# Performance work log

Hardware: AMD Instinct MI355X
Metric: run time of the kernel (lower is better)

The kernel has to match this reference:

```python
import jax, jax.numpy as jnp
import numpy as np

EPS = 1e-5
TAU = 0.1

def _bn(x, g, b):
    # BatchNorm1d in training mode: batch statistics (biased variance)
    mu = jnp.mean(x, axis=0, keepdims=True)
    var = jnp.var(x, axis=0, keepdims=True)
    return (x - mu) * jax.lax.rsqrt(var + EPS) * g + b

def setup_inputs():
    key = jax.random.key(0)
    ks = jax.random.split(key, 8)
    B, D, H, L, P, C, ND, NP = 32768, 2048, 1024, 384, 192, 10, 2, 2
    s = 0.02
    u = jax.random.uniform(ks[7], (B, NP), minval=1e-6, maxval=1.0 - 1e-6)
    return {
        'x': jax.random.normal(ks[0], (B, D), dtype=jnp.float32),
        'W_pre': jax.random.normal(ks[1], (H, D), dtype=jnp.float32) * s,
        'b_pre': jnp.zeros((H,), jnp.float32),
        'g_pre': jnp.ones((H,), jnp.float32),
        'be_pre': jnp.zeros((H,), jnp.float32),
        'W_disc': jax.random.normal(ks[2], (L, H), dtype=jnp.float32) * s,
        'b_disc': jnp.zeros((L,), jnp.float32),
        'g_disc': jnp.ones((L,), jnp.float32),
        'be_disc': jnp.zeros((L,), jnp.float32),
        'W_dfc': jax.random.normal(ks[3], (ND, L), dtype=jnp.float32) * s,
        'b_dfc': jnp.zeros((ND,), jnp.float32),
        'W_sw': jax.random.normal(ks[4], (NP, L), dtype=jnp.float32) * s,
        'b_sw': jnp.zeros((NP,), jnp.float32),
        'W1': jax.random.normal(ks[5], (NP, P, H), dtype=jnp.float32) * s,
        'b1': jnp.zeros((NP, P), jnp.float32),
        'W2': jax.random.normal(ks[6], (NP, C, P), dtype=jnp.float32) * s,
        'b2': jnp.zeros((NP, C), jnp.float32),
        'gumbel_noise': -jnp.log(-jnp.log(u)),
    }

def reference(x, W_pre, b_pre, g_pre, be_pre, W_disc, b_disc, g_disc, be_disc,
              W_dfc, b_dfc, W_sw, b_sw, W1, b1, W2, b2, gumbel_noise):
    # pre_classifier: Linear + BN + ReLU
    feature = jax.nn.relu(_bn(x @ W_pre.T + b_pre, g_pre, be_pre))
    # GRL is identity in forward
    dp = jax.nn.relu(_bn(feature @ W_disc.T + b_disc, g_disc, be_disc))
    dom = dp @ W_dfc.T + b_dfc                      # [B, num_domains]
    sw = jax.nn.relu(dp @ W_sw.T + b_sw)            # [B, n_partition]
    gum = jax.nn.softmax((sw + gumbel_noise) / TAU, axis=-1)  # soft gumbel-softmax
    idx = jnp.argmax(gum, axis=-1)                  # [B] routing decision
    # compute both (tiny) experts densely, then select per sample (faithful math,
    # avoids per-sample gather of full weight matrices)
    h_all = jax.nn.relu(jnp.einsum('bd,epd->bep', feature, W1) + b1)  # [B,E,P]
    o_all = jnp.einsum('bep,ecp->bec', h_all, W2) + b2                # [B,E,C]
    out = jnp.take_along_axis(o_all, idx[:, None, None], axis=1)[:, 0]  # [B,C]
    # original: sum_p gum[b,p] * stacked (stacked has one entry) == out * sum(gum)
    cop = out * jnp.sum(gum, axis=-1, keepdims=True)
    return cop, dom, idx
```

## Files before the change

### kernel.cpp

```cpp
#include <hip/hip_runtime.h>
#include <math.h>

#define kB 32768
#define kD 2048
#define kH 1024
#define kL 384
#define kP 192
#define kC 10
#define kNP 2
#define kND 2
#define kNCAT 768
#define kTAU 0.1f
#define kEPS 1e-5f
#define NPART 256
#define SCALE 64.0f
#define INV_SC2 (1.0f / 4096.0f)

typedef _Float16 f16x8 __attribute__((ext_vector_type(8)));
typedef _Float16 f16x4 __attribute__((ext_vector_type(4)));
typedef float f32x4 __attribute__((ext_vector_type(4)));

#define WAITVM4   asm volatile("s_waitcnt vmcnt(4)" ::: "memory")
#define WAITVM0   asm volatile("s_waitcnt vmcnt(0)" ::: "memory")
#define WAITLGKM0 asm volatile("s_waitcnt lgkmcnt(0)" ::: "memory")

__device__ __forceinline__ void gll16(const unsigned short* g, unsigned short* l)
{
    __builtin_amdgcn_global_load_lds(
        (const __attribute__((address_space(1))) unsigned int*)g,
        (__attribute__((address_space(3))) unsigned int*)l, 16, 0, 0);
}

__device__ __host__ __forceinline__ int wkey(int r)
{
    return (r & 1) | ((r & 2) << 1) | ((r & 4) >> 1);
}

__global__ __launch_bounds__(256)
void split_pack(const float* __restrict__ in, unsigned short* __restrict__ out, int K)
{
    const int row = blockIdx.x;
    const int t = threadIdx.x;
    const int s = wkey(row & 7);
    const float* ir = in + (size_t)row * K;
    unsigned short* orow = out + (size_t)row * (K * 2);
    for (int k0 = t * 4; k0 < K; k0 += 1024) {
        const float4 v = *(const float4*)&ir[k0];
        const float a0 = v.x * SCALE, a1 = v.y * SCALE, a2 = v.z * SCALE, a3 = v.w * SCALE;
        const _Float16 h0 = (_Float16)a0, h1 = (_Float16)a1, h2 = (_Float16)a2, h3 = (_Float16)a3;
        const _Float16 l0 = (_Float16)(a0 - (float)h0), l1 = (_Float16)(a1 - (float)h1);
        const _Float16 l2 = (_Float16)(a2 - (float)h2), l3 = (_Float16)(a3 - (float)h3);
        const f16x4 hi = {h0, h1, h2, h3};
        const f16x4 lo = {l0, l1, l2, l3};
        const int kb = k0 >> 5, kk = k0 & 31;
        const int c = kk >> 3, off = kk & 7;
        *(f16x4*)&orow[kb * 64 + ((c ^ s) << 3) + off]       = hi;
        *(f16x4*)&orow[kb * 64 + (((c ^ 4) ^ s) << 3) + off] = lo;
    }
}

template<int KDIM, int TILEN, bool BN>
__global__ __launch_bounds__(512, 1)
void gemm_fused(const float* __restrict__ Afp,
                const unsigned short* __restrict__ Bpk,
                const float* __restrict__ bnsc, const float* __restrict__ bnsh,
                float* __restrict__ C, const int N, const int gridX,
                float* __restrict__ psum, float* __restrict__ psumsq, const int statN)
{
    constexpr int NKB = KDIM / 32;
    constexpr int NI = TILEN / 64;
    constexpr int BG = TILEN / 64;
    __shared__ __align__(16) unsigned short As_[2][256 * 64];
    __shared__ __align__(16) unsigned short Bs_[2][TILEN * 64];
    __shared__ float sScL[BN ? KDIM : 1];
    __shared__ float sShL[BN ? KDIM : 1];

    const int t = threadIdx.x;
    const int lane = t & 63;
    const int w = t >> 6;
    const int wr = w >> 2, wc = w & 3;
    const int lr = lane & 15, lg = lane >> 4;
    const int ca = (lg ^ wkey(lane & 7)) * 8;

    const int nwg = gridDim.x;
    const int chunk = nwg >> 3;
    const int bid = blockIdx.x;
    const int logical = (bid & 7) * chunk + (bid >> 3);
    const int bx = logical % gridX, by = logical / gridX;
    const int m0 = by * 256, n0 = bx * TILEN;

    const int arow = t >> 1;
    const int akh = t & 1;
    const int skey = wkey(arow & 7);
    const int c0 = akh * 2, c1 = akh * 2 + 1;
    const float* aSrc = Afp + (size_t)(m0 + arow) * KDIM + akh * 16;

    const size_t bstride = (size_t)NKB * 64;
    const unsigned short* bG[BG];
    int bLoff[BG];
#pragma unroll
    for (int it = 0; it < BG; ++it) {
        const int Q = (w * BG + it) * 64 + lane;
        bG[it] = Bpk + (size_t)(n0 + (Q >> 3)) * bstride + (Q & 7) * 8;
        bLoff[it] = (w * BG + it) * 512;
    }

    f32x4 acc[8][NI];
#pragma unroll
    for (int mi = 0; mi < 8; ++mi)
#pragma unroll
        for (int ni = 0; ni < NI; ++ni) acc[mi][ni] = (f32x4){0.f, 0.f, 0.f, 0.f};

    float4 av0[4], av1[4];

    auto issueA = [&](float4 (&av)[4], int kb) {
        const int kt = kb * 32;
#pragma unroll
        for (int j = 0; j < 4; ++j)
            av[j] = *(const float4*)&aSrc[kt + j * 4];
    };

    auto gllB = [&](int kb, int buf) {
#pragma unroll
        for (int it = 0; it < BG; ++it)
            gll16(bG[it] + (size_t)kb * 64, &Bs_[buf][bLoff[it]]);
    };

    auto writeA = [&](const float4 (&av)[4], int buf, int tile) {
        const int kt = tile * 32 + akh * 16;
        float v[16];
#pragma unroll
        for (int j = 0; j < 4; ++j) {
            float4 a = av[j];
            if constexpr (BN) {
                const float4 sc = *(const float4*)&sScL[kt + j * 4];
                const float4 sh = *(const float4*)&sShL[kt + j * 4];
                a.x = fmaxf(fmaf(a.x, sc.x, sh.x), 0.f);
                a.y = fmaxf(fmaf(a.y, sc.y, sh.y), 0.f);
                a.z = fmaxf(fmaf(a.z, sc.z, sh.z), 0.f);
                a.w = fmaxf(fmaf(a.w, sc.w, sh.w), 0.f);
            } else {
                a.x *= SCALE; a.y *= SCALE; a.z *= SCALE; a.w *= SCALE;
            }
            v[j * 4 + 0] = a.x; v[j * 4 + 1] = a.y;
            v[j * 4 + 2] = a.z; v[j * 4 + 3] = a.w;
        }
        f16x8 hi[2], lo[2];
#pragma unroll
        for (int h = 0; h < 2; ++h)
#pragma unroll
            for (int i = 0; i < 8; ++i) {
                const float x = v[h * 8 + i];
                const _Float16 hh = (_Float16)x;
                hi[h][i] = hh;
                lo[h][i] = (_Float16)(x - (float)hh);
            }
        unsigned short* dst = &As_[buf][arow * 64];
        *(f16x8*)&dst[(c0 ^ skey) * 8]       = hi[0];
        *(f16x8*)&dst[(c1 ^ skey) * 8]       = hi[1];
        *(f16x8*)&dst[((c0 ^ 4) ^ skey) * 8] = lo[0];
        *(f16x8*)&dst[((c1 ^ 4) ^ skey) * 8] = lo[1];
    };

    auto body = [&](int kb, const float4 (&avW)[4], float4 (&avI)[4]) {
        const int cur = kb & 1, nxt = cur ^ 1;
        if (kb + 1 < NKB) {
            writeA(avW, nxt, kb + 1);
            gllB(kb + 1, nxt);
        }
        __builtin_amdgcn_sched_barrier(0);
        if (kb + 2 < NKB) issueA(avI, kb + 2);

        f16x8 bh[NI], bl[NI];
#pragma unroll
        for (int ni = 0; ni < NI; ++ni) {
            const unsigned short* bb = &Bs_[cur][(wc * (16 * NI) + ni * 16 + lr) * 64];
            bh[ni] = *(const f16x8*)&bb[ca];
            bl[ni] = *(const f16x8*)&bb[ca ^ 32];
        }
#pragma unroll
        for (int mi = 0; mi < 8; ++mi) {
            const unsigned short* ab = &As_[cur][(wr * 128 + mi * 16 + lr) * 64];
            const f16x8 ah = *(const f16x8*)&ab[ca];
            const f16x8 al = *(const f16x8*)&ab[ca ^ 32];
#pragma unroll
            for (int ni = 0; ni < NI; ++ni)
                acc[mi][ni] = __builtin_amdgcn_mfma_f32_16x16x32_f16(ah, bh[ni], acc[mi][ni], 0, 0, 0);
#pragma unroll
            for (int ni = 0; ni < NI; ++ni)
                acc[mi][ni] = __builtin_amdgcn_mfma_f32_16x16x32_f16(ah, bl[ni], acc[mi][ni], 0, 0, 0);
#pragma unroll
            for (int ni = 0; ni < NI; ++ni)
                acc[mi][ni] = __builtin_amdgcn_mfma_f32_16x16x32_f16(al, bh[ni], acc[mi][ni], 0, 0, 0);
        }
        if (kb + 1 < NKB) {
            if (kb + 2 < NKB) { WAITVM4; } else { WAITVM0; }
            WAITLGKM0;
            __builtin_amdgcn_sched_barrier(0);
            __builtin_amdgcn_s_barrier();
            __builtin_amdgcn_sched_barrier(0);
        }
    };

    if constexpr (BN) {
        if (t < KDIM / 4) {
            ((float4*)sScL)[t] = ((const float4*)bnsc)[t];
            ((float4*)sShL)[t] = ((const float4*)bnsh)[t];
        }
        __syncthreads();
    }
    issueA(av0, 0);
    gllB(0, 0);
    __builtin_amdgcn_sched_barrier(0);
    issueA(av1, 1);
    writeA(av0, 0, 0);
    WAITVM4;
    WAITLGKM0;
    __builtin_amdgcn_sched_barrier(0);
    __builtin_amdgcn_s_barrier();
    __builtin_amdgcn_sched_barrier(0);

    for (int kb = 0; kb < NKB; kb += 2) {
        body(kb,     av1, av0);
        body(kb + 1, av0, av1);
    }

#pragma unroll
    for (int mi = 0; mi < 8; ++mi)
#pragma unroll
        for (int j = 0; j < 4; ++j) {
            const int row = m0 + wr * 128 + mi * 16 + lg * 4 + j;
            float* cr = C + (size_t)row * N + n0 + wc * (16 * NI) + lr;
#pragma unroll
            for (int ni = 0; ni < NI; ++ni) cr[ni * 16] = acc[mi][ni][j];
        }

#pragma unroll
    for (int ni = 0; ni < NI; ++ni) {
        float s = 0.f, sq = 0.f;
#pragma unroll
        for (int mi = 0; mi < 8; ++mi)
#pragma unroll
            for (int j = 0; j < 4; ++j) {
                const float v = acc[mi][ni][j];
                s += v;
                sq = fmaf(v, v, sq);
            }
        s  += __shfl_xor(s, 16);  s  += __shfl_xor(s, 32);
        sq += __shfl_xor(sq, 16); sq += __shfl_xor(sq, 32);
        const int col = n0 + wc * (16 * NI) + ni * 16 + lr;
        if (lane < 16 && col < statN) {
            psum[(size_t)(by * 2 + wr) * statN + col]   = s;
            psumsq[(size_t)(by * 2 + wr) * statN + col] = sq;
        }
    }
}

__global__ __launch_bounds__(256)
void colstat_finalize(const float* __restrict__ psum, const float* __restrict__ psumsq,
                      int ncols, const float* __restrict__ g, const float* __restrict__ be,
                      float* __restrict__ scale, float* __restrict__ shift,
                      float inv_sc, float outsc)
{
    const int c = blockIdx.x * 256 + threadIdx.x;
    if (c >= ncols) return;
    float s = 0.f, sq = 0.f;
    for (int i = 0; i < NPART; ++i) {
        s  += psum[(size_t)i * ncols + c];
        sq += psumsq[(size_t)i * ncols + c];
    }
    const float mup = s * (1.f / kB);
    const float var = (sq * (1.f / kB) - mup * mup) * inv_sc * inv_sc;
    const float scl = outsc * g[c] * rsqrtf(var + kEPS) * inv_sc;
    scale[c] = scl;
    shift[c] = fmaf(-mup, scl, outsc * be[c]);
}

__global__ __launch_bounds__(256)
void tail_kernel(const float* __restrict__ Z2,
                 const float* __restrict__ scale2, const float* __restrict__ shift2,
                 const float* __restrict__ W_dfc, const float* __restrict__ b_dfc,
                 const float* __restrict__ W_sw, const float* __restrict__ b_sw,
                 const float* __restrict__ b1, const float* __restrict__ W2,
                 const float* __restrict__ b2, const float* __restrict__ noise,
                 float* __restrict__ out)
{
    __shared__ float sWdfc[kND * kL];
    __shared__ float sWsw[kNP * kL];
    __shared__ float sW2[kNP * kC * kP];
    __shared__ float sb1[kNP * kP];
    __shared__ float sScale[kL];
    __shared__ float sShift[kL];
    const int t = threadIdx.x;
    for (int i = t; i < kND * kL; i += 256) sWdfc[i] = W_dfc[i];
    for (int i = t; i < kNP * kL; i += 256) sWsw[i] = W_sw[i];
    for (int i = t; i < kNP * kC * kP; i += 256) sW2[i] = W2[i];
    for (int i = t; i < kNP * kP; i += 256) sb1[i] = b1[i];
    for (int i = t; i < kL; i += 256) { sScale[i] = scale2[i]; sShift[i] = shift2[i]; }
    __syncthreads();

    const int lane = t & 63;
    const int b = blockIdx.x * 4 + (t >> 6);
    const float* z = Z2 + (size_t)b * kNCAT;

    float d0 = 0.f, d1 = 0.f, s0 = 0.f, s1 = 0.f;
#pragma unroll
    for (int j = 0; j < 6; ++j) {
        const int k = lane + j * 64;
        const float dp = fmaxf(fmaf(z[k], sScale[k], sShift[k]), 0.f);
        d0 = fmaf(dp, sWdfc[k],      d0);
        d1 = fmaf(dp, sWdfc[kL + k], d1);
        s0 = fmaf(dp, sWsw[k],       s0);
        s1 = fmaf(dp, sWsw[kL + k],  s1);
    }
#pragma unroll
    for (int off = 32; off; off >>= 1) {
        d0 += __shfl_xor(d0, off);
        d1 += __shfl_xor(d1, off);
        s0 += __shfl_xor(s0, off);
        s1 += __shfl_xor(s1, off);
    }
    d0 += b_dfc[0];
    d1 += b_dfc[1];

    const float sw0 = fmaxf(s0 + b_sw[0], 0.f);
    const float sw1 = fmaxf(s1 + b_sw[1], 0.f);
    const float l0 = (sw0 + noise[(size_t)b * 2 + 0]) * (1.f / kTAU);
    const float l1 = (sw1 + noise[(size_t)b * 2 + 1]) * (1.f / kTAU);
    const float mx = fmaxf(l0, l1);
    const float e0 = expf(l0 - mx), e1 = expf(l1 - mx);
    const float inv = 1.f / (e0 + e1);
    const float sgum = e0 * inv + e1 * inv;
    const int idx = (l1 > l0) ? 1 : 0;

    const float* zh = z + kL + idx * kP;
    const float h0 = fmaxf(fmaf(zh[lane],       INV_SC2, sb1[idx * kP + lane]),       0.f);
    const float h1 = fmaxf(fmaf(zh[lane + 64],  INV_SC2, sb1[idx * kP + lane + 64]),  0.f);
    const float h2 = fmaxf(fmaf(zh[lane + 128], INV_SC2, sb1[idx * kP + lane + 128]), 0.f);

    float* cop  = out;
    float* dom  = out + (size_t)kB * kC;
    float* idxo = dom + (size_t)kB * kND;

#pragma unroll
    for (int c = 0; c < kC; ++c) {
        const float* wv = &sW2[(idx * kC + c) * kP];
        float oc = h0 * wv[lane] + h1 * wv[lane + 64] + h2 * wv[lane + 128];
#pragma unroll
        for (int off = 32; off; off >>= 1) oc += __shfl_xor(oc, off);
        if (lane == c) cop[(size_t)b * kC + c] = (oc + b2[idx * kC + c]) * sgum;
    }
    if (lane == 0) {
        dom[(size_t)b * 2 + 0] = d0;
        dom[(size_t)b * 2 + 1] = d1;
        idxo[b] = (float)idx;
    }
}

extern "C" void kernel_launch(void* const* d_in, const int* in_sizes, int n_in,
                              void* d_out, int out_size, void* d_ws, size_t ws_size,
                              hipStream_t stream)
{
    const float* x       = (const float*)d_in[0];
    const float* W_pre   = (const float*)d_in[1];
    const float* g_pre   = (const float*)d_in[3];
    const float* be_pre  = (const float*)d_in[4];
    const float* W_disc  = (const float*)d_in[5];
    const float* g_disc  = (const float*)d_in[7];
    const float* be_disc = (const float*)d_in[8];
    const float* W_dfc   = (const float*)d_in[9];
    const float* b_dfc   = (const float*)d_in[10];
    const float* W_sw    = (const float*)d_in[11];
    const float* b_sw    = (const float*)d_in[12];
    const float* W1      = (const float*)d_in[13];
    const float* b1      = (const float*)d_in[14];
    const float* W2      = (const float*)d_in[15];
    const float* b2      = (const float*)d_in[16];
    const float* noise   = (const float*)d_in[17];

    char* wsb = (char*)d_ws;
    unsigned short* Wps = (unsigned short*)wsb;
    unsigned short* Ws2 = (unsigned short*)(wsb + (size_t)1024 * 4096 * 2);
    float* Z1 = (float*)(wsb + (size_t)1024 * 4096 * 2 + (size_t)768 * 2048 * 2);
    float* Z2 = Z1 + (size_t)kB * kH;
    float* psum1  = Z2 + (size_t)kB * kNCAT;
    float* psq1   = psum1 + (size_t)NPART * kH;
    float* psum2  = psq1 + (size_t)NPART * kH;
    float* psq2   = psum2 + (size_t)NPART * kL;
    float* scale1 = psq2 + (size_t)NPART * kL;
    float* shift1 = scale1 + kH;
    float* scale2 = shift1 + kH;
    float* shift2 = scale2 + kL;
    float* out    = (float*)d_out;

    split_pack<<<dim3(kH), 256, 0, stream>>>(W_pre, Wps, kD);
    split_pack<<<dim3(kL), 256, 0, stream>>>(W_disc, Ws2, kH);
    split_pack<<<dim3(kNP * kP), 256, 0, stream>>>(W1, Ws2 + (size_t)kL * (2 * kH), kH);
    gemm_fused<kD, 256, false><<<dim3(4 * 128), 512, 0, stream>>>(
        x, Wps, nullptr, nullptr, Z1, kH, 4, psum1, psq1, kH);
    colstat_finalize<<<dim3(kH / 256), 256, 0, stream>>>(psum1, psq1, kH, g_pre, be_pre,
                                                         scale1, shift1, INV_SC2, SCALE);
    gemm_fused<kH, 128, true><<<dim3(6 * 128), 512, 0, stream>>>(
        Z1, Ws2, scale1, shift1, Z2, kNCAT, 6, psum2, psq2, kL);
    colstat_finalize<<<dim3((kL + 255) / 256), 256, 0, stream>>>(psum2, psq2, kL, g_disc, be_disc,
                                                                 scale2, shift2, INV_SC2, 1.0f);
    tail_kernel<<<dim3(kB / 4), 256, 0, stream>>>(Z2, scale2, shift2, W_dfc, b_dfc,
                                                  W_sw, b_sw, b1, W2, b2, noise, out);
}
```

Measured before the change: 671.7 us.

## Restructure GEMM main loop into two-phase ping-pong schedule with priority hints

Measured after the change: 719.6 us. 1.07x slower.

```diff
diff --git a/kernel.cpp b/kernel.cpp
--- a/kernel.cpp
+++ b/kernel.cpp
@@ -20,9 +20,10 @@
 typedef _Float16 f16x4 __attribute__((ext_vector_type(4)));
 typedef float f32x4 __attribute__((ext_vector_type(4)));
 
-#define WAITVM4   asm volatile("s_waitcnt vmcnt(4)" ::: "memory")
 #define WAITVM0   asm volatile("s_waitcnt vmcnt(0)" ::: "memory")
 #define WAITLGKM0 asm volatile("s_waitcnt lgkmcnt(0)" ::: "memory")
+#define SB0       __builtin_amdgcn_sched_barrier(0)
+#define BAR       __builtin_amdgcn_s_barrier()
 
 __device__ __forceinline__ void gll16(const unsigned short* g, unsigned short* l)
 {
@@ -72,8 +73,8 @@
     constexpr int BG = TILEN / 64;
     __shared__ __align__(16) unsigned short As_[2][256 * 64];
     __shared__ __align__(16) unsigned short Bs_[2][TILEN * 64];
-    __shared__ float sScL[BN ? KDIM : 1];
-    __shared__ float sShL[BN ? KDIM : 1];
+    __shared__ float sScL[BN ? KDIM : 4];
+    __shared__ float sShL[BN ? KDIM : 4];
 
     const int t = threadIdx.x;
     const int lane = t & 63;
@@ -111,9 +112,9 @@
 #pragma unroll
         for (int ni = 0; ni < NI; ++ni) acc[mi][ni] = (f32x4){0.f, 0.f, 0.f, 0.f};
 
-    float4 av0[4], av1[4];
-
-    auto issueA = [&](float4 (&av)[4], int kb) {
+    float4 av[4];
+
+    auto issueA = [&](int kb) {
         const int kt = kb * 32;
 #pragma unroll
         for (int j = 0; j < 4; ++j)
@@ -126,7 +127,7 @@
             gll16(bG[it] + (size_t)kb * 64, &Bs_[buf][bLoff[it]]);
     };
 
-    auto writeA = [&](const float4 (&av)[4], int buf, int tile) {
+    auto writeA = [&](int buf, int tile) {
         const int kt = tile * 32 + akh * 16;
         float v[16];
 #pragma unroll
@@ -162,16 +163,29 @@
         *(f16x8*)&dst[((c1 ^ 4) ^ skey) * 8] = lo[1];
     };
 
-    auto body = [&](int kb, const float4 (&avW)[4], float4 (&avI)[4]) {
-        const int cur = kb & 1, nxt = cur ^ 1;
-        if (kb + 1 < NKB) {
-            writeA(avW, nxt, kb + 1);
-            gllB(kb + 1, nxt);
-        }
-        __builtin_amdgcn_sched_barrier(0);
-        if (kb + 2 < NKB) issueA(avI, kb + 2);
-
-        f16x8 bh[NI], bl[NI];
+    if constexpr (BN) {
+        if (t < KDIM / 4) {
+            ((float4*)sScL)[t] = ((const float4*)bnsc)[t];
+            ((float4*)sShL)[t] = ((const float4*)bnsh)[t];
+        }
+        __syncthreads();
+    }
+    issueA(0);
+    gllB(0, 0);
+    SB0;
+    if constexpr (BG == 4) { asm volatile("s_waitcnt vmcnt(4)" ::: "memory"); }
+    else                   { asm volatile("s_waitcnt vmcnt(2)" ::: "memory"); }
+    writeA(0, 0);
+    WAITLGKM0;
+    WAITVM0;
+    SB0;
+    BAR;
+
+    for (int s = 0; s < NKB; ++s) {
+        const int cur = s & 1, nxt = cur ^ 1;
+        const bool pf = (s + 1 < NKB);
+
+        f16x8 bh[NI], bl[NI], ah0[4], al0[4];
 #pragma unroll
         for (int ni = 0; ni < NI; ++ni) {
             const unsigned short* bb = &Bs_[cur][(wc * (16 * NI) + ni * 16 + lr) * 64];
@@ -179,50 +193,61 @@
             bl[ni] = *(const f16x8*)&bb[ca ^ 32];
         }
 #pragma unroll
-        for (int mi = 0; mi < 8; ++mi) {
+        for (int mi = 0; mi < 4; ++mi) {
             const unsigned short* ab = &As_[cur][(wr * 128 + mi * 16 + lr) * 64];
-            const f16x8 ah = *(const f16x8*)&ab[ca];
-            const f16x8 al = *(const f16x8*)&ab[ca ^ 32];
-#pragma unroll
-            for (int ni = 0; ni < NI; ++ni)
-                acc[mi][ni] = __builtin_amdgcn_mfma_f32_16x16x32_f16(ah, bh[ni], acc[mi][ni], 0, 0, 0);
-#pragma unroll
-            for (int ni = 0; ni < NI; ++ni)
-                acc[mi][ni] = __builtin_amdgcn_mfma_f32_16x16x32_f16(ah, bl[ni], acc[mi][ni], 0, 0, 0);
-#pragma unroll
-            for (int ni = 0; ni < NI; ++ni)
-                acc[mi][ni] = __builtin_amdgcn_mfma_f32_16x16x32_f16(al, bh[ni], acc[mi][ni], 0, 0, 0);
-        }
-        if (kb + 1 < NKB) {
-            if (kb + 2 < NKB) { WAITVM4; } else { WAITVM0; }
-            WAITLGKM0;
-            __builtin_amdgcn_sched_barrier(0);
-            __builtin_amdgcn_s_barrier();
-            __builtin_amdgcn_sched_barrier(0);
-        }
-    };
-
-    if constexpr (BN) {
-        if (t < KDIM / 4) {
-            ((float4*)sScL)[t] = ((const float4*)bnsc)[t];
-            ((float4*)sShL)[t] = ((const float4*)bnsh)[t];
-        }
-        __syncthreads();
-    }
-    issueA(av0, 0);
-    gllB(0, 0);
-    __builtin_amdgcn_sched_barrier(0);
-    issueA(av1, 1);
-    writeA(av0, 0, 0);
-    WAITVM4;
-    WAITLGKM0;
-    __builtin_amdgcn_sched_barrier(0);
-    __builtin_amdgcn_s_barrier();
-    __builtin_amdgcn_sched_barrier(0);
-
-    for (int kb = 0; kb < NKB; kb += 2) {
-        body(kb,     av1, av0);
-        body(kb + 1, av0, av1);
+            ah0[mi] = *(const f16x8*)&ab[ca];
+            al0[mi] = *(const f16x8*)&ab[ca ^ 32];
+        }
+        if (pf) {
+            issueA(s + 1);
+            gllB(s + 1, nxt);
+        }
+        SB0;
+        BAR;
+        WAITLGKM0;
+        SB0;
+        __builtin_amdgcn_s_setprio(1);
+#pragma unroll
+        for (int mi = 0; mi < 4; ++mi)
+#pragma unroll
+            for (int ni = 0; ni < NI; ++ni) {
+                acc[mi][ni] = __builtin_amdgcn_mfma_f32_16x16x32_f16(ah0[mi], bh[ni], acc[mi][ni], 0, 0, 0);
+                acc[mi][ni] = __builtin_amdgcn_mfma_f32_16x16x32_f16(ah0[mi], bl[ni], acc[mi][ni], 0, 0, 0);
+                acc[mi][ni] = __builtin_amdgcn_mfma_f32_16x16x32_f16(al0[mi], bh[ni], acc[mi][ni], 0, 0, 0);
+            }
+        __builtin_amdgcn_s_setprio(0);
+        SB0;
+        BAR;
+
+        f16x8 ah1[4], al1[4];
+#pragma unroll
+        for (int mi = 0; mi < 4; ++mi) {
+            const unsigned short* ab = &As_[cur][(wr * 128 + (mi + 4) * 16 + lr) * 64];
+            ah1[mi] = *(const f16x8*)&ab[ca];
+            al1[mi] = *(const f16x8*)&ab[ca ^ 32];
+        }
+        if (pf) {
+            if constexpr (BG == 4) { asm volatile("s_waitcnt vmcnt(4)" ::: "memory"); }
+            else                   { asm volatile("s_waitcnt vmcnt(2)" ::: "memory"); }
+            writeA(nxt, s + 1);
+        }
+        SB0;
+        WAITLGKM0;
+        SB0;
+        BAR;
+        __builtin_amdgcn_s_setprio(1);
+#pragma unroll
+        for (int mi = 0; mi < 4; ++mi)
+#pragma unroll
+            for (int ni = 0; ni < NI; ++ni) {
+                acc[mi + 4][ni] = __builtin_amdgcn_mfma_f32_16x16x32_f16(ah1[mi], bh[ni], acc[mi + 4][ni], 0, 0, 0);
+                acc[mi + 4][ni] = __builtin_amdgcn_mfma_f32_16x16x32_f16(ah1[mi], bl[ni], acc[mi + 4][ni], 0, 0, 0);
+                acc[mi + 4][ni] = __builtin_amdgcn_mfma_f32_16x16x32_f16(al1[mi], bh[ni], acc[mi + 4][ni], 0, 0, 0);
+            }
+        __builtin_amdgcn_s_setprio(0);
+        SB0;
+        if (pf) { WAITVM0; }
+        BAR;
     }
 
 #pragma unroll
```
